# Optimization experiments

Measured on AMD Instinct MI355X. Metric: run time of the kernel, lower is better.

## Reference

```python
import jax, jax.numpy as jnp
import numpy as np

N = 8192  # must be divisible by 4
C = 2048


def setup_inputs() -> dict:
    key = jax.random.key(0)
    k1, k2 = jax.random.split(key, 2)
    x = jax.random.normal(k1, (N, C), dtype=jnp.float32)
    att_w = jax.random.normal(k2, (1, C), dtype=jnp.float32) * 0.02  # nn.Linear(2048,1) weight
    att_b = jnp.zeros((1,), dtype=jnp.float32)                        # nn.Linear bias
    return {"x": x, "att_w": att_w, "att_b": att_b}


def reference(x, att_w, att_b):
    n, c = x.shape
    s = n // 4  # stride
    # attention scores [N,1], split into 4 segments and normalize per segment
    w = x @ att_w.T + att_b                      # [N,1]
    w = w.reshape(4, s, 1)
    w = w / w.sum(axis=1, keepdims=True)         # per-segment normalization
    # attention-pooled centers: sum over each segment -> [4, C]
    centers = (x.reshape(4, s, c) * w).sum(axis=1)
    x_new = jnp.concatenate([x, centers], axis=0)  # [N+4, C]

    # build adjacency: identity, center block all-ones, segment<->center links
    adj = jnp.eye(n + 4, dtype=x.dtype)
    adj = adj.at[n:, n:].set(1.0)
    for i in range(4):
        adj = adj.at[i * s:(i + 1) * s, n + i].set(1.0)
        adj = adj.at[n + i, i * s:(i + 1) * s].set(1.0)

    # gen_adj: D = deg^-1/2 ; adj_out = (A @ diag(D)).T @ diag(D) = D * A^T * D
    d = adj.sum(axis=1) ** -0.5                  # [N+4]
    adj = (adj * d[None, :]).T * d[None, :]      # degree normalization as broadcast scale
    return x_new, adj
```

## Files before the change

kernel.cpp:

```cpp
#include <hip/hip_runtime.h>

constexpr int N = 8192;
constexpr int C = 2048;
constexpr int ND = N + 4;
constexpr size_t XNEW_ELEMS = (size_t)ND * C;
constexpr size_t ADJ_ELEMS  = (size_t)ND * ND;
constexpr int ATT_BLOCKS = 1024;
constexpr int KB_PER_SEG = ATT_BLOCKS / 4;

#define C_DIAG 0.5f
#define C_LINK 0.015609764f
#define C_BLK  (1.0f / 2052.0f)

typedef float f32x4 __attribute__((ext_vector_type(4)));

__global__ __launch_bounds__(256) void k_adj_nz(float* __restrict__ adj) {
    const int t = blockIdx.x * 256 + threadIdx.x;
    if (t < N) {
        adj[(size_t)t * ND + t] = C_DIAG;
        adj[(size_t)t * ND + N + (t >> 11)] = C_LINK;
    } else if (t < N + 4 * 2052) {
        const int u = t - N;
        const int i = u / 2052;
        const int j = u - i * 2052;
        const size_t rowb = (size_t)(N + i) * ND;
        if (j < 2048) adj[rowb + i * 2048 + j] = C_LINK;
        else          adj[rowb + N + (j - 2048)] = C_BLK;
    }
}

template <bool USE_WS>
__global__ __launch_bounds__(256) void k_att(const float* __restrict__ x,
                                             const float* __restrict__ attw,
                                             const float* __restrict__ attb,
                                             float* __restrict__ xnew,
                                             float* __restrict__ part,
                                             float* __restrict__ wpart) {
    __shared__ float lnum[4][C];
    __shared__ float lw[4];

    const int tid  = threadIdx.x;
    const int wave = tid >> 6;
    const int lane = tid & 63;
    const int row0 = blockIdx.x * 8;
    const int seg  = blockIdx.x >> 8;
    const float bias = attb[0];

    f32x4 wv[8];
#pragma unroll
    for (int q = 0; q < 8; ++q)
        wv[q] = reinterpret_cast<const f32x4*>(attw)[lane + 64 * q];

    float acc[32];
#pragma unroll
    for (int k = 0; k < 32; ++k) acc[k] = 0.0f;
    float wacc = 0.0f;

    for (int r = 0; r < 2; ++r) {
        const int row = row0 + wave * 2 + r;
        const f32x4* xrow = reinterpret_cast<const f32x4*>(x + (size_t)row * C);
        f32x4* orow = reinterpret_cast<f32x4*>(xnew + (size_t)row * C);

        f32x4 xv[8];
        float dot = 0.0f;
#pragma unroll
        for (int q = 0; q < 8; ++q) {
            xv[q] = xrow[lane + 64 * q];
            dot += xv[q].x * wv[q].x + xv[q].y * wv[q].y +
                   xv[q].z * wv[q].z + xv[q].w * wv[q].w;
        }
#pragma unroll
        for (int off = 32; off > 0; off >>= 1) dot += __shfl_xor(dot, off, 64);
        const float wrow = dot + bias;
        wacc += wrow;
#pragma unroll
        for (int q = 0; q < 8; ++q) {
            acc[4 * q + 0] += wrow * xv[q].x;
            acc[4 * q + 1] += wrow * xv[q].y;
            acc[4 * q + 2] += wrow * xv[q].z;
            acc[4 * q + 3] += wrow * xv[q].w;
            orow[lane + 64 * q] = xv[q];
        }
    }

#pragma unroll
    for (int q = 0; q < 8; ++q) {
        f32x4 s;
        s.x = acc[4 * q];     s.y = acc[4 * q + 1];
        s.z = acc[4 * q + 2]; s.w = acc[4 * q + 3];
        reinterpret_cast<f32x4*>(&lnum[wave][0])[lane + 64 * q] = s;
    }
    if (lane == 0) lw[wave] = wacc;
    __syncthreads();

    const f32x4* l0 = reinterpret_cast<const f32x4*>(&lnum[0][0]);
    const f32x4* l1 = reinterpret_cast<const f32x4*>(&lnum[1][0]);
    const f32x4* l2 = reinterpret_cast<const f32x4*>(&lnum[2][0]);
    const f32x4* l3 = reinterpret_cast<const f32x4*>(&lnum[3][0]);
#pragma unroll
    for (int c4 = tid; c4 < C / 4; c4 += 256) {
        f32x4 s = l0[c4] + l1[c4] + l2[c4] + l3[c4];
        if constexpr (USE_WS) {
            reinterpret_cast<f32x4*>(part + (size_t)blockIdx.x * C)[c4] = s;
        } else {
            float* dst = &xnew[(size_t)(N + seg) * C + 4 * c4];
            atomicAdd(dst + 0, s.x); atomicAdd(dst + 1, s.y);
            atomicAdd(dst + 2, s.z); atomicAdd(dst + 3, s.w);
        }
    }
    if (tid == 0) {
        const float wb = lw[0] + lw[1] + lw[2] + lw[3];
        if constexpr (USE_WS) wpart[blockIdx.x] = wb;
        else                  atomicAdd(&wpart[seg], wb);
    }
}

__global__ __launch_bounds__(256) void k_centers(const float* __restrict__ part,
                                                 const float* __restrict__ wpart,
                                                 float* __restrict__ xnew) {
    const int idx = blockIdx.x * 256 + threadIdx.x;
    const int seg = idx >> 11;
    const int c   = idx & 2047;
    float wsum = 0.0f;
#pragma unroll 8
    for (int k = 0; k < KB_PER_SEG; ++k) wsum += wpart[seg * KB_PER_SEG + k];
    float s = 0.0f;
#pragma unroll 8
    for (int k = 0; k < KB_PER_SEG; ++k)
        s += part[(size_t)(seg * KB_PER_SEG + k) * C + c];
    xnew[(size_t)(N + seg) * C + c] = s / wsum;
}

__global__ __launch_bounds__(256) void k_zero(float* __restrict__ xnew,
                                              float* __restrict__ wseg) {
    int idx = blockIdx.x * 256 + threadIdx.x;
    if (idx < 4 * C) xnew[(size_t)N * C + idx] = 0.0f;
    if (idx < 4) wseg[idx] = 0.0f;
}
__global__ __launch_bounds__(256) void k_div(float* __restrict__ xnew,
                                             const float* __restrict__ wseg) {
    int idx = blockIdx.x * 256 + threadIdx.x;
    if (idx < 4 * C) xnew[(size_t)N * C + idx] /= wseg[idx >> 11];
}

extern "C" void kernel_launch(void* const* d_in, const int* in_sizes, int n_in,
                              void* d_out, int out_size, void* d_ws, size_t ws_size,
                              hipStream_t stream) {
    const float* x    = (const float*)d_in[0];
    const float* attw = (const float*)d_in[1];
    const float* attb = (const float*)d_in[2];
    float* xnew = (float*)d_out;
    float* adj  = (float*)d_out + XNEW_ELEMS;

    hipMemsetAsync(adj, 0, ADJ_ELEMS * sizeof(float), stream);
    k_adj_nz<<<(N + 4 * 2052 + 255) / 256, 256, 0, stream>>>(adj);

    const size_t ws_need = (2048 + (size_t)ATT_BLOCKS * C) * sizeof(float);
    if (ws_size >= ws_need) {
        float* wpart = (float*)d_ws;
        float* part  = (float*)d_ws + 2048;
        k_att<true><<<ATT_BLOCKS, 256, 0, stream>>>(x, attw, attb, xnew, part, wpart);
        k_centers<<<32, 256, 0, stream>>>(part, wpart, xnew);
    } else {
        float* wseg = (float*)d_ws;
        k_zero<<<32, 256, 0, stream>>>(xnew, wseg);
        k_att<false><<<ATT_BLOCKS, 256, 0, stream>>>(x, attw, attb, xnew, nullptr, wseg);
        k_div<<<32, 256, 0, stream>>>(xnew, wseg);
    }
}
```

Measured before the change: 102.9 us.

## Fuse adjacency memset and nonzero writes into one vectorized 2D fill kernel

Replaces the full-matrix memset followed by a scatter kernel with a single kernel that computes each adjacency value and writes it with float4 stores. This removes one pass of scattered writes and a separate operation. The attention kernel also processes 16 rows per block, halving the number of partial sums that the centers reduction has to combine. Risks are some per-element compute in the fill and lower occupancy from fewer attention blocks.

```diff
diff --git a/kernel.cpp b/kernel.cpp
--- a/kernel.cpp
+++ b/kernel.cpp
@@ -4,9 +4,6 @@
 constexpr int C = 2048;
 constexpr int ND = N + 4;
 constexpr size_t XNEW_ELEMS = (size_t)ND * C;
-constexpr size_t ADJ_ELEMS  = (size_t)ND * ND;
-constexpr int ATT_BLOCKS = 1024;
-constexpr int KB_PER_SEG = ATT_BLOCKS / 4;
 
 #define C_DIAG 0.5f
 #define C_LINK 0.015609764f
@@ -14,19 +11,28 @@
 
 typedef float f32x4 __attribute__((ext_vector_type(4)));
 
-__global__ __launch_bounds__(256) void k_adj_nz(float* __restrict__ adj) {
-    const int t = blockIdx.x * 256 + threadIdx.x;
-    if (t < N) {
-        adj[(size_t)t * ND + t] = C_DIAG;
-        adj[(size_t)t * ND + N + (t >> 11)] = C_LINK;
-    } else if (t < N + 4 * 2052) {
-        const int u = t - N;
-        const int i = u / 2052;
-        const int j = u - i * 2052;
-        const size_t rowb = (size_t)(N + i) * ND;
-        if (j < 2048) adj[rowb + i * 2048 + j] = C_LINK;
-        else          adj[rowb + N + (j - 2048)] = C_BLK;
+__global__ __launch_bounds__(256) void k_adj2d(float* __restrict__ adj) {
+    const int row   = blockIdx.y;
+    const int chunk = blockIdx.x * 256 + threadIdx.x;
+    if (chunk >= ND / 4) return;
+    f32x4 v;
+    if (row < N) {
+        const int  dgc = row >> 2;
+        const int  r3  = row & 3;
+        const int  sg  = row >> 11;
+        const bool dg  = (chunk == dgc);
+        const bool lk  = (chunk == 2048);
+        v.x = (dg && r3 == 0) ? C_DIAG : ((lk && sg == 0) ? C_LINK : 0.0f);
+        v.y = (dg && r3 == 1) ? C_DIAG : ((lk && sg == 1) ? C_LINK : 0.0f);
+        v.z = (dg && r3 == 2) ? C_DIAG : ((lk && sg == 2) ? C_LINK : 0.0f);
+        v.w = (dg && r3 == 3) ? C_DIAG : ((lk && sg == 3) ? C_LINK : 0.0f);
+    } else {
+        const int a = row - N;
+        const float f = (chunk == 2048) ? C_BLK
+                      : (((chunk >> 9) == a) ? C_LINK : 0.0f);
+        v.x = f; v.y = f; v.z = f; v.w = f;
     }
+    reinterpret_cast<f32x4*>(adj + (size_t)row * ND)[chunk] = v;
 }
 
 template <bool USE_WS>
@@ -42,8 +48,8 @@
     const int tid  = threadIdx.x;
     const int wave = tid >> 6;
     const int lane = tid & 63;
-    const int row0 = blockIdx.x * 8;
-    const int seg  = blockIdx.x >> 8;
+    const int row0 = blockIdx.x * 16;
+    const int seg  = blockIdx.x >> 7;
     const float bias = attb[0];
 
     f32x4 wv[8];
@@ -56,8 +62,8 @@
     for (int k = 0; k < 32; ++k) acc[k] = 0.0f;
     float wacc = 0.0f;
 
-    for (int r = 0; r < 2; ++r) {
-        const int row = row0 + wave * 2 + r;
+    for (int r = 0; r < 4; ++r) {
+        const int row = row0 + wave * 4 + r;
         const f32x4* xrow = reinterpret_cast<const f32x4*>(x + (size_t)row * C);
         f32x4* orow = reinterpret_cast<f32x4*>(xnew + (size_t)row * C);
 
@@ -123,11 +129,10 @@
     const int c   = idx & 2047;
     float wsum = 0.0f;
 #pragma unroll 8
-    for (int k = 0; k < KB_PER_SEG; ++k) wsum += wpart[seg * KB_PER_SEG + k];
+    for (int k = 0; k < 128; ++k) wsum += wpart[seg * 128 + k];
     float s = 0.0f;
 #pragma unroll 8
-    for (int k = 0; k < KB_PER_SEG; ++k)
-        s += part[(size_t)(seg * KB_PER_SEG + k) * C + c];
+    for (int k = 0; k < 128; ++k) s += part[(size_t)(seg * 128 + k) * C + c];
     xnew[(size_t)(N + seg) * C + c] = s / wsum;
 }
 
@@ -152,19 +157,18 @@
     float* xnew = (float*)d_out;
     float* adj  = (float*)d_out + XNEW_ELEMS;
 
-    hipMemsetAsync(adj, 0, ADJ_ELEMS * sizeof(float), stream);
-    k_adj_nz<<<(N + 4 * 2052 + 255) / 256, 256, 0, stream>>>(adj);
+    k_adj2d<<<dim3(9, ND), 256, 0, stream>>>(adj);
 
-    const size_t ws_need = (2048 + (size_t)ATT_BLOCKS * C) * sizeof(float);
+    const size_t ws_need = (1024 + (size_t)512 * C) * sizeof(float);
     if (ws_size >= ws_need) {
         float* wpart = (float*)d_ws;
-        float* part  = (float*)d_ws + 2048;
-        k_att<true><<<ATT_BLOCKS, 256, 0, stream>>>(x, attw, attb, xnew, part, wpart);
+        float* part  = (float*)d_ws + 1024;
+        k_att<true><<<N / 16, 256, 0, stream>>>(x, attw, attb, xnew, part, wpart);
         k_centers<<<32, 256, 0, stream>>>(part, wpart, xnew);
     } else {
         float* wseg = (float*)d_ws;
         k_zero<<<32, 256, 0, stream>>>(xnew, wseg);
-        k_att<false><<<ATT_BLOCKS, 256, 0, stream>>>(x, attw, attb, xnew, nullptr, wseg);
+        k_att<false><<<N / 16, 256, 0, stream>>>(x, attw, attb, xnew, nullptr, wseg);
         k_div<<<32, 256, 0, stream>>>(xnew, wseg);
     }
 }
```

After: 100.1 us. 1.03x faster.
